# Performance work log

Hardware: AMD Instinct MI355X
Metric: run time of the kernel (lower is better)

Reference implementation:

```python
import jax, jax.numpy as jnp
import numpy as np

N = 16384  # n_nodes
D = 64     # feature dim


def setup_inputs() -> dict:
    key = jax.random.key(0)
    kx, ka = jax.random.split(key)
    x = jax.random.normal(kx, (N, D), dtype=jnp.float32)
    # original code only tests adj[idx] == 1, so 0/1 int entries are faithful
    adj = jax.random.randint(ka, (N, N), 0, 2, dtype=jnp.int32)
    return {"x": x, "adj": adj}


def reference(x, adj):
    # GraphPool: for each node, sum its own feature vector plus the feature
    # vectors of all neighbors j with adj[i, j] == 1.
    # Vectorized: out = adj @ x + x  (dense binary SpMM + self term).
    a = (adj == 1).astype(x.dtype)  # [N, N]
    return jnp.matmul(a, x) + x     # [N, D]
```

## Files before the change

### kernel.cpp

```cpp
#include <hip/hip_runtime.h>

#define NN 16384
#define DD 64

typedef _Float16 f16x8 __attribute__((ext_vector_type(8)));
typedef short    s16x8 __attribute__((ext_vector_type(8)));
typedef float    f32x4 __attribute__((ext_vector_type(4)));
typedef int      i32x4 __attribute__((ext_vector_type(4)));
typedef unsigned u32;

__global__ __launch_bounds__(256) void prep_adj(const int* __restrict__ adj,
                                                u32* __restrict__ pk) {
    const u32 tid = blockIdx.x * 256 + threadIdx.x;
    for (int it = 0; it < 16; ++it) {
        size_t g = (size_t)it * (2048 * 256) + tid;
        const i32x4* src = (const i32x4*)(adj + g * 32);
        u32 b = 0;
#pragma unroll
        for (int j = 0; j < 8; ++j) {
            i32x4 v = __builtin_nontemporal_load(src + j);
            b |= (u32)(v.x != 0) << (j * 4 + 0);
            b |= (u32)(v.y != 0) << (j * 4 + 1);
            b |= (u32)(v.z != 0) << (j * 4 + 2);
            b |= (u32)(v.w != 0) << (j * 4 + 3);
        }
        pk[g] = b;
    }
}

__global__ __launch_bounds__(256) void prep_x(const float* __restrict__ x,
                                              _Float16* __restrict__ ws) {
    __shared__ float sx[32][65];
    const int tid = threadIdx.x;
    const int t   = blockIdx.x;
    {
        int r  = tid >> 3;
        int c8 = (tid & 7) * 8;
        const float* src = x + ((size_t)t * 32 + r) * DD + c8;
        f32x4 a = *(const f32x4*)src;
        f32x4 b = *(const f32x4*)(src + 4);
#pragma unroll
        for (int j = 0; j < 4; ++j) { sx[r][c8 + j] = a[j]; sx[r][c8 + 4 + j] = b[j]; }
    }
    __syncthreads();
    const int l = tid & 63;
    const int c = tid >> 6;
    const int q = l >> 4;
    const int m = l & 15;
    f16x8 v;
#pragma unroll
    for (int j = 0; j < 8; ++j)
        v[j] = (_Float16)sx[q * 8 + j][c * 16 + m];
    *(f16x8*)(ws + (((size_t)t * 256 + c * 64 + l) * 8)) = v;
}

__global__ __launch_bounds__(256) void graphpool_gemm(const u32* __restrict__ pk,
                                                      const float* __restrict__ x,
                                                      const _Float16* __restrict__ xs,
                                                      float* __restrict__ out) {
    __shared__ _Float16 sB[2][8192];

    const int tid = threadIdx.x;
    const int w   = tid >> 6;
    const int l   = tid & 63;
    const int q   = l >> 4;
    const int m   = l & 15;
    const int row16 = blockIdx.x * 64 + w * 16;

    const i32x4* aptr = (const i32x4*)pk + (size_t)(row16 + m) * 128;

    f32x4 acc[4];
#pragma unroll
    for (int c = 0; c < 4; ++c) acc[c] = (f32x4){0.f, 0.f, 0.f, 0.f};

    i32x4 areg[2];
    f16x8 sreg[4];

    auto loadA = [&](int n, int buf) { areg[buf] = aptr[n]; };
    auto stageRead = [&](int n) {
        const f16x8* src = (const f16x8*)xs + (size_t)n * 1024;
#pragma unroll
        for (int p = 0; p < 4; ++p) sreg[p] = src[p * 256 + tid];
    };
    auto stageWrite = [&](int buf) {
        f16x8* dst = (f16x8*)sB[buf];
#pragma unroll
        for (int p = 0; p < 4; ++p) dst[p * 256 + tid] = sreg[p];
    };

    stageRead(0);
    loadA(0, 0);
    stageWrite(0);
    __syncthreads();

    constexpr int NCH = NN / 128;
    for (int n = 0; n < NCH; ++n) {
        const int buf = n & 1;
        const bool pf = (n + 1 < NCH);
        if (pf) { stageRead(n + 1); loadA(n + 1, buf ^ 1); }
#pragma unroll
        for (int s = 0; s < 4; ++s) {
            u32 byte = (((u32)areg[buf][s]) >> (q * 8)) & 0xffu;
            s16x8 ai;
#pragma unroll
            for (int j = 0; j < 8; ++j)
                ai[j] = ((byte >> j) & 1u) ? (short)0x3C00 : (short)0;
            f16x8 af = __builtin_bit_cast(f16x8, ai);
#pragma unroll
            for (int c = 0; c < 4; ++c) {
                f16x8 bf = *(const f16x8*)&sB[buf][((s * 4 + c) * 64 + l) * 8];
                acc[c] = __builtin_amdgcn_mfma_f32_16x16x32_f16(af, bf, acc[c], 0, 0, 0);
            }
        }
        if (pf) stageWrite(buf ^ 1);
        __syncthreads();
    }

#pragma unroll
    for (int c = 0; c < 4; ++c) {
#pragma unroll
        for (int r = 0; r < 4; ++r) {
            int row = row16 + q * 4 + r;
            int col = c * 16 + m;
            size_t off = (size_t)row * DD + col;
            out[off] = acc[c][r] + x[off];
        }
    }
}

__global__ void graphpool_fallback(const int* __restrict__ adj,
                                   const float* __restrict__ x,
                                   float* __restrict__ out) {
    int i = blockIdx.x;
    int d = threadIdx.x;
    float acc = x[(size_t)i * DD + d];
    const int* row = adj + (size_t)i * NN;
    for (int j = 0; j < NN; ++j)
        if (row[j]) acc += x[(size_t)j * DD + d];
    out[(size_t)i * DD + d] = acc;
}

extern "C" void kernel_launch(void* const* d_in, const int* in_sizes, int n_in,
                              void* d_out, int out_size, void* d_ws, size_t ws_size,
                              hipStream_t stream) {
    const float* x   = (const float*)d_in[0];
    const int*   adj = (const int*)d_in[1];
    float*       out = (float*)d_out;

    const size_t xs_bytes = (size_t)NN * DD * sizeof(_Float16);
    const size_t pk_bytes = (size_t)NN * (NN / 32) * sizeof(u32);
    if (ws_size >= xs_bytes + pk_bytes) {
        _Float16* xs = (_Float16*)d_ws;
        u32*      pk = (u32*)((char*)d_ws + xs_bytes);
        prep_adj<<<2048, 256, 0, stream>>>(adj, pk);
        prep_x<<<512, 256, 0, stream>>>(x, xs);
        graphpool_gemm<<<256, 256, 0, stream>>>(pk, x, xs, out);
    } else {
        graphpool_fallback<<<NN, 64, 0, stream>>>(adj, x, out);
    }
}
```

Baseline: 1.681 ms.

## Pack adjacency with wave ballots and coalesced loads, remap bit layout in GEMM

The adjacency bit-packing kernel now has each wave load contiguous 512-int segments with fully coalesced 16-byte loads, double-buffered, and builds the packed words with __ballot instead of per-thread serial 32-element reads. This produces a permuted bit layout, so the GEMM kernel's A-fragment decode is rewritten to pull bits from four words and loads A two vectors at a time across chunk pairs. The aim is to cut the cost of streaming the 1 GiB int adjacency matrix, which dominates runtime, at the price of more intricate bit-index bookkeeping that must exactly match between packer and consumer.

```diff
diff --git a/kernel.cpp b/kernel.cpp
--- a/kernel.cpp
+++ b/kernel.cpp
@@ -8,23 +8,52 @@
 typedef float    f32x4 __attribute__((ext_vector_type(4)));
 typedef int      i32x4 __attribute__((ext_vector_type(4)));
 typedef unsigned u32;
-
-__global__ __launch_bounds__(256) void prep_adj(const int* __restrict__ adj,
+typedef unsigned long long u64;
+
+__global__ __launch_bounds__(256) void pack_adj(const int* __restrict__ adj,
                                                 u32* __restrict__ pk) {
-    const u32 tid = blockIdx.x * 256 + threadIdx.x;
-    for (int it = 0; it < 16; ++it) {
-        size_t g = (size_t)it * (2048 * 256) + tid;
-        const i32x4* src = (const i32x4*)(adj + g * 32);
-        u32 b = 0;
-#pragma unroll
-        for (int j = 0; j < 8; ++j) {
-            i32x4 v = __builtin_nontemporal_load(src + j);
-            b |= (u32)(v.x != 0) << (j * 4 + 0);
-            b |= (u32)(v.y != 0) << (j * 4 + 1);
-            b |= (u32)(v.z != 0) << (j * 4 + 2);
-            b |= (u32)(v.w != 0) << (j * 4 + 3);
+    const int tid = threadIdx.x;
+    const int w   = tid >> 6;
+    const int l   = tid & 63;
+    const int g   = blockIdx.x * 4 + w;
+
+    i32x4 v[2][2];
+    auto segLoad = [&](int it, int buf) {
+        const size_t seg = (size_t)g * 128 + it;
+        const i32x4* p = (const i32x4*)(adj + seg * 512) + l;
+        v[buf][0] = p[0];
+        v[buf][1] = p[64];
+    };
+
+    segLoad(0, 0);
+    for (int it = 0; it < 128; ++it) {
+        const int buf = it & 1;
+        if (it + 1 < 128) segLoad(it + 1, buf ^ 1);
+
+        const u64 b00 = __ballot(v[buf][0].x != 0);
+        const u64 b01 = __ballot(v[buf][0].y != 0);
+        const u64 b02 = __ballot(v[buf][0].z != 0);
+        const u64 b03 = __ballot(v[buf][0].w != 0);
+        const u64 b10 = __ballot(v[buf][1].x != 0);
+        const u64 b11 = __ballot(v[buf][1].y != 0);
+        const u64 b12 = __ballot(v[buf][1].z != 0);
+        const u64 b13 = __ballot(v[buf][1].w != 0);
+
+        auto half = [&](u64 b) { return (l & 1) ? (u32)(b >> 32) : (u32)b; };
+        const u32 e0 = half(b00), e1 = half(b01), e2 = half(b02), e3 = half(b03);
+        const u32 f0 = half(b10), f1 = half(b11), f2 = half(b12), f3 = half(b13);
+        const u32 x01 = ((l >> 1) & 1) ? e1 : e0;
+        const u32 x23 = ((l >> 1) & 1) ? e3 : e2;
+        const u32 xe  = ((l >> 2) & 1) ? x23 : x01;
+        const u32 y01 = ((l >> 1) & 1) ? f1 : f0;
+        const u32 y23 = ((l >> 1) & 1) ? f3 : f2;
+        const u32 yf  = ((l >> 2) & 1) ? y23 : y01;
+        const u32 val = ((l >> 3) & 1) ? yf : xe;
+
+        if (l < 16) {
+            const size_t seg = (size_t)g * 128 + it;
+            pk[seg * 16 + l] = val;
         }
-        pk[g] = b;
     }
 }
 
@@ -67,16 +96,19 @@
     const int m   = l & 15;
     const int row16 = blockIdx.x * 64 + w * 16;
 
-    const i32x4* aptr = (const i32x4*)pk + (size_t)(row16 + m) * 128;
+    const i32x4* aptr = (const i32x4*)(pk + (size_t)(row16 + m) * 512);
 
     f32x4 acc[4];
 #pragma unroll
     for (int c = 0; c < 4; ++c) acc[c] = (f32x4){0.f, 0.f, 0.f, 0.f};
 
-    i32x4 areg[2];
+    i32x4 av[2][2];
     f16x8 sreg[4];
 
-    auto loadA = [&](int n, int buf) { areg[buf] = aptr[n]; };
+    auto loadA = [&](int np, int buf) {
+        av[buf][0] = aptr[np * 2];
+        av[buf][1] = aptr[np * 2 + 1];
+    };
     auto stageRead = [&](int n) {
         const f16x8* src = (const f16x8*)xs + (size_t)n * 1024;
 #pragma unroll
@@ -88,23 +120,22 @@
         for (int p = 0; p < 4; ++p) dst[p * 256 + tid] = sreg[p];
     };
 
-    stageRead(0);
-    loadA(0, 0);
-    stageWrite(0);
-    __syncthreads();
-
-    constexpr int NCH = NN / 128;
-    for (int n = 0; n < NCH; ++n) {
+    auto doChunk = [&](int n, u32 D0, u32 D1, u32 D2, u32 D3) {
         const int buf = n & 1;
-        const bool pf = (n + 1 < NCH);
-        if (pf) { stageRead(n + 1); loadA(n + 1, buf ^ 1); }
+        const bool pf = (n + 1 < 128);
+        if (pf) stageRead(n + 1);
 #pragma unroll
         for (int s = 0; s < 4; ++s) {
-            u32 byte = (((u32)areg[buf][s]) >> (q * 8)) & 0xffu;
+            const u32 bb = 8 * s + 2 * q;
             s16x8 ai;
-#pragma unroll
-            for (int j = 0; j < 8; ++j)
-                ai[j] = ((byte >> j) & 1u) ? (short)0x3C00 : (short)0;
+            ai[0] = ((D0 >> bb) & 1u)       ? (short)0x3C00 : (short)0;
+            ai[1] = ((D1 >> bb) & 1u)       ? (short)0x3C00 : (short)0;
+            ai[2] = ((D2 >> bb) & 1u)       ? (short)0x3C00 : (short)0;
+            ai[3] = ((D3 >> bb) & 1u)       ? (short)0x3C00 : (short)0;
+            ai[4] = ((D0 >> (bb + 1)) & 1u) ? (short)0x3C00 : (short)0;
+            ai[5] = ((D1 >> (bb + 1)) & 1u) ? (short)0x3C00 : (short)0;
+            ai[6] = ((D2 >> (bb + 1)) & 1u) ? (short)0x3C00 : (short)0;
+            ai[7] = ((D3 >> (bb + 1)) & 1u) ? (short)0x3C00 : (short)0;
             f16x8 af = __builtin_bit_cast(f16x8, ai);
 #pragma unroll
             for (int c = 0; c < 4; ++c) {
@@ -114,6 +145,19 @@
         }
         if (pf) stageWrite(buf ^ 1);
         __syncthreads();
+    };
+
+    stageRead(0);
+    loadA(0, 0);
+    stageWrite(0);
+    __syncthreads();
+
+    for (int np = 0; np < 64; ++np) {
+        const int ab = np & 1;
+        if (np + 1 < 64) loadA(np + 1, ab ^ 1);
+        const i32x4 a0 = av[ab][0], a1 = av[ab][1];
+        doChunk(2 * np,     (u32)a0.x, (u32)a0.z, (u32)a1.x, (u32)a1.z);
+        doChunk(2 * np + 1, (u32)a0.y, (u32)a0.w, (u32)a1.y, (u32)a1.w);
     }
 
 #pragma unroll
@@ -152,7 +196,7 @@
     if (ws_size >= xs_bytes + pk_bytes) {
         _Float16* xs = (_Float16*)d_ws;
         u32*      pk = (u32*)((char*)d_ws + xs_bytes);
-        prep_adj<<<2048, 256, 0, stream>>>(adj, pk);
+        pack_adj<<<1024, 256, 0, stream>>>(adj, pk);
         prep_x<<<512, 256, 0, stream>>>(x, xs);
         graphpool_gemm<<<256, 256, 0, stream>>>(pk, x, xs, out);
     } else {
```

After: 1.569 ms. 6.7% less time.
